# Kernel optimization log

Hardware: AMD Instinct MI355X
Metric: run time of the kernel (lower is better)

The kernel has to match this reference:

```python
import jax, jax.numpy as jnp
import numpy as np

D = 160          # SDF grid resolution (D1=D2=D3=D)
LEVEL = 0.0      # marching_cubes(-sdf, level=-0) == level 0 on s = -sdf
N_SMOOTH = 2
LAMBD = 1.0


def _extract_mesh_np():
    """Host-side isosurface extraction (mirrors the module's CPU round-trip).
    Uses marching tetrahedra (6-tet cube decomposition) in place of skimage's
    lewiner marching cubes; topo_correct (undefined in source) is identity.
    Returns (verts [V,3] f32 in normalized coords, faces [F,3] i32, edges [E,2] i32).
    """
    xs = np.arange(D, dtype=np.float32)
    X, Y, Z = np.meshgrid(xs, xs, xs, indexing='ij')
    ctr = (D - 1) / 2.0
    sdf = np.sqrt((X - ctr) ** 2 + (Y - ctr) ** 2 + (Z - ctr) ** 2) - 0.35 * D
    sdf = sdf + 3.0 * np.sin(0.20 * X) * np.sin(0.17 * Y) * np.sin(0.23 * Z)
    s = (-sdf).astype(np.float32)  # extract level-0 isosurface of -sdf
    sflat = s.ravel()
    Ng = D ** 3

    corner_off = [(0, 0, 0), (1, 0, 0), (1, 1, 0), (0, 1, 0),
                  (0, 0, 1), (1, 0, 1), (1, 1, 1), (0, 1, 1)]
    b = np.arange(D - 1)
    BX, BY, BZ = np.meshgrid(b, b, b, indexing='ij')
    BX, BY, BZ = BX.ravel(), BY.ravel(), BZ.ravel()
    gid8 = [((BX + dx) * D + (BY + dy)) * D + (BZ + dz) for dx, dy, dz in corner_off]
    val8 = [sflat[g] for g in gid8]

    TETS = [(0, 5, 1, 6), (0, 1, 2, 6), (0, 2, 3, 6),
            (0, 3, 7, 6), (0, 7, 4, 6), (0, 4, 5, 6)]
    TE = [(0, 1), (0, 2), (0, 3), (1, 2), (1, 3), (2, 3)]  # tet edges
    CASE_TRIS = {1: [(0, 1, 2)], 14: [(0, 1, 2)],
                 2: [(0, 3, 4)], 13: [(0, 3, 4)],
                 4: [(1, 3, 5)], 11: [(1, 3, 5)],
                 8: [(2, 4, 5)], 7: [(2, 4, 5)],
                 3: [(1, 3, 4), (1, 4, 2)], 12: [(1, 3, 4), (1, 4, 2)],
                 5: [(0, 3, 5), (0, 5, 2)], 10: [(0, 3, 5), (0, 5, 2)],
                 6: [(0, 4, 5), (0, 5, 1)], 9: [(0, 4, 5), (0, 5, 1)]}
    bitw = np.array([1, 2, 4, 8])

    tri_keys = []
    for tet in TETS:
        tv = np.stack([val8[c] for c in tet], 1)  # [Nc,4] corner values
        tg = np.stack([gid8[c] for c in tet], 1)  # [Nc,4] corner grid ids
        case = (tv < LEVEL).astype(np.int64) @ bitw
        for c, tris in CASE_TRIS.items():
            sel = np.nonzero(case == c)[0]
            if sel.size == 0:
                continue
            g = tg[sel]
            for tri in tris:
                cols = []
                for e in tri:
                    i, j = TE[e]
                    lo = np.minimum(g[:, i], g[:, j])
                    hi = np.maximum(g[:, i], g[:, j])
                    cols.append(lo * Ng + hi)  # canonical grid-edge key
                tri_keys.append(np.stack(cols, 1))
    tris = np.concatenate(tri_keys, 0)  # [F,3] edge keys
    uk, inv = np.unique(tris, return_inverse=True)
    faces = inv.reshape(-1, 3).astype(np.int32)
    ga = uk // Ng
    gb = uk % Ng
    pa = np.stack(np.unravel_index(ga, (D, D, D)), 1).astype(np.float32)
    pb = np.stack(np.unravel_index(gb, (D, D, D)), 1).astype(np.float32)
    sa = sflat[ga]
    sb = sflat[gb]
    t = ((LEVEL - sa) / (sb - sa)).astype(np.float32)
    verts = pa + t[:, None] * (pb - pa)
    verts = (2.0 * verts - np.float32(D)) / np.float32(D)  # (2v-[D1,D2,D3])/D
    e = np.concatenate([faces[:, [0, 1]], faces[:, [1, 2]], faces[:, [2, 0]]], 0)
    e = np.unique(np.sort(e, 1), axis=0).astype(np.int32)
    return verts.astype(np.float32), faces, e


def setup_inputs() -> dict:
    verts, faces, edges = _extract_mesh_np()
    return {
        'v': jnp.asarray(verts)[None],      # [1,V,3]
        'edges': jnp.asarray(edges),        # [E,2] unique undirected mesh edges
        'faces': jnp.asarray(faces)[None],  # [1,F,3]
    }


def reference(v, edges, faces):
    # Uniform laplacian smoothing: v <- v + lambd * (mean_neighbor(v) - v), x2
    V = v.shape[1]
    src = jnp.concatenate([edges[:, 0], edges[:, 1]])
    dst = jnp.concatenate([edges[:, 1], edges[:, 0]])
    x = v[0]
    deg = jax.ops.segment_sum(jnp.ones(src.shape[0], x.dtype), src, num_segments=V)
    inv_deg = 1.0 / jnp.maximum(deg, 1.0)
    for _ in range(N_SMOOTH):
        nbr = jax.ops.segment_sum(x[dst], src, num_segments=V)
        x = x + LAMBD * (nbr * inv_deg[:, None] - x)
    return x, faces[0]
```

## Files before the change

kernel.cpp:

```cpp
#include <hip/hip_runtime.h>
#include <stdint.h>

#define K_ELL 32
#define K_OVF 16
#define TBS   1024
#define RNG_LOG 11
#define RNG   2048
#define BAND  2048
#define RW    (RNG + BAND)
#define BS    256
#define UA    6
#define UN    6
#define UF    4

__global__ void prep_kernel(const int2* __restrict__ edges, int* __restrict__ offs_a,
                            int* __restrict__ cntN, int* __restrict__ cntF,
                            int* __restrict__ deg_ovf, int E, int V) {
    int i = blockIdx.x * blockDim.x + threadIdx.x;
    if (i <= E) {
        if (i < E) {
            int lo = (i == 0) ? 0 : edges[i - 1].x + 1;
            int hi = edges[i].x;
            for (int a = lo; a <= hi; a++) offs_a[a] = i;
        } else {
            for (int a = edges[E - 1].x + 1; a <= V; a++) offs_a[a] = E;
        }
    }
    if (i < V) deg_ovf[i] = 0;
    if (i <= RNG) cntF[i] = 0;
    if (i == 0) cntN[0] = 0;
}

__global__ __launch_bounds__(TBS) void build_kernel(
        const int2* __restrict__ edges, const int* __restrict__ offs_a,
        int* __restrict__ cntN, int* __restrict__ cntF, int* __restrict__ deg_ovf,
        int* __restrict__ adjN, int* __restrict__ adjF, int* __restrict__ adj_ovf,
        const int* __restrict__ faces, float* __restrict__ out_f,
        const float* __restrict__ v, float4* __restrict__ v4,
        int E, int V, int F3, int NBb) {
    if ((int)blockIdx.x >= NBb) {
        int t = (blockIdx.x - NBb) * TBS + threadIdx.x;
        int T = (gridDim.x - NBb) * TBS;
        if ((((uintptr_t)out_f | (uintptr_t)faces) & 15) == 0) {
            int n4 = F3 >> 2;
            const int4* f4 = (const int4*)faces;
            float4* o4 = (float4*)out_f;
            for (int j = t; j < n4; j += T) {
                int4 a = f4[j];
                o4[j] = make_float4((float)a.x, (float)a.y, (float)a.z, (float)a.w);
            }
            for (int j = (n4 << 2) + t; j < F3; j += T) out_f[j] = (float)faces[j];
        } else {
            for (int j = t; j < F3; j += T) out_f[j] = (float)faces[j];
        }
        if (((uintptr_t)v & 15) == 0) {
            const float4* vv = (const float4*)v;
            int n4v = V >> 2;
            for (int q = t; q < n4v; q += T) {
                float4 a = vv[3 * q], b = vv[3 * q + 1], c = vv[3 * q + 2];
                v4[4 * q + 0] = make_float4(a.x, a.y, a.z, 0.f);
                v4[4 * q + 1] = make_float4(a.w, b.x, b.y, 0.f);
                v4[4 * q + 2] = make_float4(b.z, b.w, c.x, 0.f);
                v4[4 * q + 3] = make_float4(c.y, c.z, c.w, 0.f);
            }
            for (int u = (n4v << 2) + t; u < V; u += T)
                v4[u] = make_float4(v[3 * u], v[3 * u + 1], v[3 * u + 2], 0.f);
        } else {
            for (int u = t; u < V; u += T)
                v4[u] = make_float4(v[3 * u], v[3 * u + 1], v[3 * u + 2], 0.f);
        }
        return;
    }
    __shared__ int cnt[RW];
    const int v0   = blockIdx.x << RNG_LOG;
    const int vEnd = min(v0 + RNG, V);
    for (int i = threadIdx.x; i < RW; i += TBS) cnt[i] = 0;
    const int eBeg = offs_a[v0];
    const int eEnd = offs_a[vEnd];
    __syncthreads();
    for (int i = eBeg + threadIdx.x; i < eEnd; i += TBS) {
        int2 e = edges[i];
        int rel = e.y - (v0 + 1);
        if (rel < RW) {
            int r = atomicAdd(&cnt[rel], 1);
            if (rel < RNG) { if (r < K_ELL) adjN[(size_t)r * V + e.y] = e.x; }
            else           { if (r < K_ELL) adjF[(size_t)r * V + e.y] = e.x; }
        } else {
            int r = atomicAdd(&deg_ovf[e.y], 1);
            if (r < K_OVF) adj_ovf[(size_t)r * V + e.y] = e.x;
        }
    }
    __syncthreads();
    for (int i = threadIdx.x; i < RW; i += TBS) {
        int u = v0 + 1 + i;
        if (u < V) {
            if (i < RNG) cntN[u] = cnt[i];
            else         cntF[u] = cnt[i];
        }
    }
}

template <bool PAD>
__global__ void gather_kernel(const float4* __restrict__ x4, const int2* __restrict__ edges,
                              const int* __restrict__ offs_a,
                              const int* __restrict__ cntN, const int* __restrict__ cntF,
                              const int* __restrict__ deg_ovf,
                              const int* __restrict__ adjN, const int* __restrict__ adjF,
                              const int* __restrict__ adj_ovf,
                              float* __restrict__ y, int V, int E) {
    int u = blockIdx.x * blockDim.x + threadIdx.x;
    if (u >= V) return;
    int aBeg = offs_a[u], aEnd = offs_a[u + 1];
    int cN = cntN[u], cF = cntF[u], dO = deg_ovf[u];
    int da = aEnd - aBeg;
    int kN = cN > K_ELL ? K_ELL : cN;
    int kF = cF > K_ELL ? K_ELL : cF;
    int gA[UA], gN[UN], gF[UF];
    #pragma unroll
    for (int j = 0; j < UA; ++j) gA[j] = edges[min(aBeg + j, E - 1)].y;
    #pragma unroll
    for (int k = 0; k < UN; ++k) gN[k] = adjN[(size_t)k * V + u];
    #pragma unroll
    for (int k = 0; k < UF; ++k) gF[k] = adjF[(size_t)k * V + u];
    float s0 = 0.f, s1 = 0.f, s2 = 0.f;
    #pragma unroll
    for (int j = 0; j < UA; ++j) {
        float m = (j < da) ? 1.f : 0.f;
        float4 p = x4[gA[j]];
        s0 += m * p.x; s1 += m * p.y; s2 += m * p.z;
    }
    for (int j = UA; j < da; ++j) {
        float4 p = x4[edges[aBeg + j].y];
        s0 += p.x; s1 += p.y; s2 += p.z;
    }
    #pragma unroll
    for (int k = 0; k < UN; ++k) {
        float m = (k < kN) ? 1.f : 0.f;
        float4 p = x4[(k < kN) ? gN[k] : 0];
        s0 += m * p.x; s1 += m * p.y; s2 += m * p.z;
    }
    for (int k = UN; k < kN; ++k) {
        float4 p = x4[adjN[(size_t)k * V + u]];
        s0 += p.x; s1 += p.y; s2 += p.z;
    }
    #pragma unroll
    for (int k = 0; k < UF; ++k) {
        float m = (k < kF) ? 1.f : 0.f;
        float4 p = x4[(k < kF) ? gF[k] : 0];
        s0 += m * p.x; s1 += m * p.y; s2 += m * p.z;
    }
    for (int k = UF; k < kF; ++k) {
        float4 p = x4[adjF[(size_t)k * V + u]];
        s0 += p.x; s1 += p.y; s2 += p.z;
    }
    int kO = dO > K_OVF ? K_OVF : dO;
    for (int k = 0; k < kO; ++k) {
        float4 p = x4[adj_ovf[(size_t)k * V + u]];
        s0 += p.x; s1 += p.y; s2 += p.z;
    }
    int d = da + cN + cF + dO;
    float inv = 1.0f / fmaxf((float)d, 1.0f);
    if (PAD) {
        ((float4*)y)[u] = make_float4(s0 * inv, s1 * inv, s2 * inv, 0.f);
    } else {
        y[3 * u + 0] = s0 * inv;
        y[3 * u + 1] = s1 * inv;
        y[3 * u + 2] = s2 * inv;
    }
}

extern "C" void kernel_launch(void* const* d_in, const int* in_sizes, int n_in,
                              void* d_out, int out_size, void* d_ws, size_t ws_size,
                              hipStream_t stream) {
    const float* v     = (const float*)d_in[0];
    const int2*  edges = (const int2*)d_in[1];
    const int*   faces = (const int*)d_in[2];

    const int V3 = in_sizes[0];
    const int V  = V3 / 3;
    const int E  = in_sizes[1] / 2;
    const int F3 = in_sizes[2];

    float* out_v = (float*)d_out;
    float* out_f = (float*)d_out + V3;

    float4* v4      = (float4*)d_ws;
    float4* x1      = v4 + V;
    int*    adjN    = (int*)(x1 + V);
    int*    adjF    = adjN + (size_t)K_ELL * V;
    int*    adj_ovf = adjF + (size_t)K_ELL * V;
    int*    offs_a  = adj_ovf + (size_t)K_OVF * V;
    int*    cntN    = offs_a + (V + 1);
    int*    cntF    = cntN + (V + 1);
    int*    deg_ovf = cntF + (V + 1);

    const int NBb = (V + RNG - 1) / RNG;
    const int copyElems = F3 > V ? F3 : V;
    const int NBc = (copyElems + TBS - 1) / TBS;
    const int gP  = (E + 1 + BS - 1) / BS;
    const int gV  = (V + BS - 1) / BS;

    prep_kernel<<<gP, BS, 0, stream>>>(edges, offs_a, cntN, cntF, deg_ovf, E, V);

    build_kernel<<<NBb + NBc, TBS, 0, stream>>>(edges, offs_a, cntN, cntF, deg_ovf,
                                                adjN, adjF, adj_ovf, faces, out_f,
                                                v, v4, E, V, F3, NBb);

    gather_kernel<true ><<<gV, BS, 0, stream>>>(v4, edges, offs_a, cntN, cntF, deg_ovf,
                                                adjN, adjF, adj_ovf, (float*)x1, V, E);
    gather_kernel<false><<<gV, BS, 0, stream>>>(x1, edges, offs_a, cntN, cntF, deg_ovf,
                                                adjN, adjF, adj_ovf, out_v, V, E);
}
```

Baseline: 86.52 us.

## Fuse prep into build with global atomics and stage vertex halo in LDS for gather

Drops the separate prep kernel. Offsets, faces conversion, vertex padding and adjacency construction now run in one grid-stride build kernel that uses global atomics on per-vertex counters, which a memset zeroes first. The gather kernels use 1024-thread blocks that stage a halo window of vertex positions in LDS (about 144KB) and serve in-window neighbours from there, falling back to global loads otherwise. The large LDS footprint cuts occupancy, and the global atomics may contend more than the old LDS counting.

```diff
diff --git a/kernel.cpp b/kernel.cpp
--- a/kernel.cpp
+++ b/kernel.cpp
@@ -3,130 +3,122 @@
 
 #define K_ELL 32
 #define K_OVF 16
-#define TBS   1024
-#define RNG_LOG 11
 #define RNG   2048
-#define BAND  2048
-#define RW    (RNG + BAND)
-#define BS    256
+#define RW    (RNG + RNG)
+#define BB    256
 #define UA    6
 #define UN    6
 #define UF    4
-
-__global__ void prep_kernel(const int2* __restrict__ edges, int* __restrict__ offs_a,
-                            int* __restrict__ cntN, int* __restrict__ cntF,
-                            int* __restrict__ deg_ovf, int E, int V) {
-    int i = blockIdx.x * blockDim.x + threadIdx.x;
-    if (i <= E) {
-        if (i < E) {
-            int lo = (i == 0) ? 0 : edges[i - 1].x + 1;
-            int hi = edges[i].x;
-            for (int a = lo; a <= hi; a++) offs_a[a] = i;
-        } else {
-            for (int a = edges[E - 1].x + 1; a <= V; a++) offs_a[a] = E;
-        }
-    }
-    if (i < V) deg_ovf[i] = 0;
-    if (i <= RNG) cntF[i] = 0;
-    if (i == 0) cntN[0] = 0;
-}
-
-__global__ __launch_bounds__(TBS) void build_kernel(
-        const int2* __restrict__ edges, const int* __restrict__ offs_a,
+#define GBS   1024
+#define HALO  4096
+#define SPAN  (GBS + 2 * HALO)
+#define SMEM_STG (SPAN * (int)sizeof(float4))
+
+__global__ __launch_bounds__(BB) void build_kernel(
+        const int2* __restrict__ edges, int* __restrict__ offs_a,
         int* __restrict__ cntN, int* __restrict__ cntF, int* __restrict__ deg_ovf,
         int* __restrict__ adjN, int* __restrict__ adjF, int* __restrict__ adj_ovf,
         const int* __restrict__ faces, float* __restrict__ out_f,
         const float* __restrict__ v, float4* __restrict__ v4,
-        int E, int V, int F3, int NBb) {
-    if ((int)blockIdx.x >= NBb) {
-        int t = (blockIdx.x - NBb) * TBS + threadIdx.x;
-        int T = (gridDim.x - NBb) * TBS;
-        if ((((uintptr_t)out_f | (uintptr_t)faces) & 15) == 0) {
-            int n4 = F3 >> 2;
-            const int4* f4 = (const int4*)faces;
-            float4* o4 = (float4*)out_f;
-            for (int j = t; j < n4; j += T) {
-                int4 a = f4[j];
-                o4[j] = make_float4((float)a.x, (float)a.y, (float)a.z, (float)a.w);
-            }
-            for (int j = (n4 << 2) + t; j < F3; j += T) out_f[j] = (float)faces[j];
-        } else {
-            for (int j = t; j < F3; j += T) out_f[j] = (float)faces[j];
-        }
-        if (((uintptr_t)v & 15) == 0) {
-            const float4* vv = (const float4*)v;
-            int n4v = V >> 2;
-            for (int q = t; q < n4v; q += T) {
-                float4 a = vv[3 * q], b = vv[3 * q + 1], c = vv[3 * q + 2];
-                v4[4 * q + 0] = make_float4(a.x, a.y, a.z, 0.f);
-                v4[4 * q + 1] = make_float4(a.w, b.x, b.y, 0.f);
-                v4[4 * q + 2] = make_float4(b.z, b.w, c.x, 0.f);
-                v4[4 * q + 3] = make_float4(c.y, c.z, c.w, 0.f);
-            }
-            for (int u = (n4v << 2) + t; u < V; u += T)
-                v4[u] = make_float4(v[3 * u], v[3 * u + 1], v[3 * u + 2], 0.f);
-        } else {
-            for (int u = t; u < V; u += T)
-                v4[u] = make_float4(v[3 * u], v[3 * u + 1], v[3 * u + 2], 0.f);
-        }
-        return;
-    }
-    __shared__ int cnt[RW];
-    const int v0   = blockIdx.x << RNG_LOG;
-    const int vEnd = min(v0 + RNG, V);
-    for (int i = threadIdx.x; i < RW; i += TBS) cnt[i] = 0;
-    const int eBeg = offs_a[v0];
-    const int eEnd = offs_a[vEnd];
-    __syncthreads();
-    for (int i = eBeg + threadIdx.x; i < eEnd; i += TBS) {
+        int E, int V, int F3) {
+    const int t = (int)blockIdx.x * BB + (int)threadIdx.x;
+    const int T = (int)gridDim.x * BB;
+    for (int i = t; i < E; i += T) {
         int2 e = edges[i];
-        int rel = e.y - (v0 + 1);
-        if (rel < RW) {
-            int r = atomicAdd(&cnt[rel], 1);
-            if (rel < RNG) { if (r < K_ELL) adjN[(size_t)r * V + e.y] = e.x; }
-            else           { if (r < K_ELL) adjF[(size_t)r * V + e.y] = e.x; }
+        int rel = e.y - (e.x & ~(RNG - 1)) - 1;
+        if (rel < RNG) {
+            int r = atomicAdd(&cntN[e.y], 1);
+            if (r < K_ELL) adjN[(size_t)r * V + e.y] = e.x;
+        } else if (rel < RW) {
+            int r = atomicAdd(&cntF[e.y], 1);
+            if (r < K_ELL) adjF[(size_t)r * V + e.y] = e.x;
         } else {
             int r = atomicAdd(&deg_ovf[e.y], 1);
             if (r < K_OVF) adj_ovf[(size_t)r * V + e.y] = e.x;
         }
     }
+    for (int i = t; i <= E; i += T) {
+        if (i < E) {
+            int lo = (i == 0) ? 0 : edges[i - 1].x + 1;
+            int hi = edges[i].x;
+            for (int a = lo; a <= hi; ++a) offs_a[a] = i;
+        } else {
+            int lo = (E > 0) ? edges[E - 1].x + 1 : 0;
+            for (int a = lo; a <= V; ++a) offs_a[a] = E;
+        }
+    }
+    if ((((uintptr_t)out_f | (uintptr_t)faces) & 15) == 0) {
+        int n4 = F3 >> 2;
+        const int4* f4 = (const int4*)faces;
+        float4* o4 = (float4*)out_f;
+        for (int j = t; j < n4; j += T) {
+            int4 a = f4[j];
+            o4[j] = make_float4((float)a.x, (float)a.y, (float)a.z, (float)a.w);
+        }
+        for (int j = (n4 << 2) + t; j < F3; j += T) out_f[j] = (float)faces[j];
+    } else {
+        for (int j = t; j < F3; j += T) out_f[j] = (float)faces[j];
+    }
+    if (((uintptr_t)v & 15) == 0) {
+        const float4* vv = (const float4*)v;
+        int n4v = V >> 2;
+        for (int q = t; q < n4v; q += T) {
+            float4 a = vv[3 * q], b = vv[3 * q + 1], c = vv[3 * q + 2];
+            v4[4 * q + 0] = make_float4(a.x, a.y, a.z, 0.f);
+            v4[4 * q + 1] = make_float4(a.w, b.x, b.y, 0.f);
+            v4[4 * q + 2] = make_float4(b.z, b.w, c.x, 0.f);
+            v4[4 * q + 3] = make_float4(c.y, c.z, c.w, 0.f);
+        }
+        for (int u = (n4v << 2) + t; u < V; u += T)
+            v4[u] = make_float4(v[3 * u], v[3 * u + 1], v[3 * u + 2], 0.f);
+    } else {
+        for (int u = t; u < V; u += T)
+            v4[u] = make_float4(v[3 * u], v[3 * u + 1], v[3 * u + 2], 0.f);
+    }
+}
+
+template <bool PAD>
+__global__ __launch_bounds__(GBS) void gather_staged(
+        const float4* __restrict__ x4, const int2* __restrict__ edges,
+        const int* __restrict__ offs_a,
+        const int* __restrict__ cntN, const int* __restrict__ cntF,
+        const int* __restrict__ deg_ovf,
+        const int* __restrict__ adjN, const int* __restrict__ adjF,
+        const int* __restrict__ adj_ovf,
+        float* __restrict__ y, int V, int E) {
+    extern __shared__ float4 tile[];
+    const int c0   = (int)blockIdx.x * GBS;
+    const int base = c0 - HALO;
+    const int u    = c0 + (int)threadIdx.x;
+    int aBeg = 0, da = 0, cN = 0, cF = 0, dO = 0;
+    int gA[UA], gN[UN], gF[UF];
+    if (u < V) {
+        aBeg = offs_a[u];
+        int aEnd = offs_a[u + 1];
+        da = aEnd - aBeg;
+        cN = cntN[u]; cF = cntF[u]; dO = deg_ovf[u];
+        #pragma unroll
+        for (int j = 0; j < UA; ++j) gA[j] = edges[min(aBeg + j, E - 1)].y;
+        #pragma unroll
+        for (int k = 0; k < UN; ++k) gN[k] = adjN[(size_t)k * V + u];
+        #pragma unroll
+        for (int k = 0; k < UF; ++k) gF[k] = adjF[(size_t)k * V + u];
+    }
+    for (int s = (int)threadIdx.x; s < SPAN; s += GBS) {
+        int g = base + s;
+        tile[s] = (g >= 0 && g < V) ? x4[g] : make_float4(0.f, 0.f, 0.f, 0.f);
+    }
     __syncthreads();
-    for (int i = threadIdx.x; i < RW; i += TBS) {
-        int u = v0 + 1 + i;
-        if (u < V) {
-            if (i < RNG) cntN[u] = cnt[i];
-            else         cntF[u] = cnt[i];
-        }
-    }
-}
-
-template <bool PAD>
-__global__ void gather_kernel(const float4* __restrict__ x4, const int2* __restrict__ edges,
-                              const int* __restrict__ offs_a,
-                              const int* __restrict__ cntN, const int* __restrict__ cntF,
-                              const int* __restrict__ deg_ovf,
-                              const int* __restrict__ adjN, const int* __restrict__ adjF,
-                              const int* __restrict__ adj_ovf,
-                              float* __restrict__ y, int V, int E) {
-    int u = blockIdx.x * blockDim.x + threadIdx.x;
     if (u >= V) return;
-    int aBeg = offs_a[u], aEnd = offs_a[u + 1];
-    int cN = cntN[u], cF = cntF[u], dO = deg_ovf[u];
-    int da = aEnd - aBeg;
     int kN = cN > K_ELL ? K_ELL : cN;
     int kF = cF > K_ELL ? K_ELL : cF;
-    int gA[UA], gN[UN], gF[UF];
-    #pragma unroll
-    for (int j = 0; j < UA; ++j) gA[j] = edges[min(aBeg + j, E - 1)].y;
-    #pragma unroll
-    for (int k = 0; k < UN; ++k) gN[k] = adjN[(size_t)k * V + u];
-    #pragma unroll
-    for (int k = 0; k < UF; ++k) gF[k] = adjF[(size_t)k * V + u];
     float s0 = 0.f, s1 = 0.f, s2 = 0.f;
     #pragma unroll
     for (int j = 0; j < UA; ++j) {
+        int g = (j < da) ? gA[j] : u;
         float m = (j < da) ? 1.f : 0.f;
-        float4 p = x4[gA[j]];
+        unsigned r = (unsigned)(g - base);
+        float4 p = (r < (unsigned)SPAN) ? tile[r] : x4[g];
         s0 += m * p.x; s1 += m * p.y; s2 += m * p.z;
     }
     for (int j = UA; j < da; ++j) {
@@ -135,8 +127,10 @@
     }
     #pragma unroll
     for (int k = 0; k < UN; ++k) {
+        int g = (k < kN) ? gN[k] : u;
         float m = (k < kN) ? 1.f : 0.f;
-        float4 p = x4[(k < kN) ? gN[k] : 0];
+        unsigned r = (unsigned)(g - base);
+        float4 p = (r < (unsigned)SPAN) ? tile[r] : x4[g];
         s0 += m * p.x; s1 += m * p.y; s2 += m * p.z;
     }
     for (int k = UN; k < kN; ++k) {
@@ -145,8 +139,10 @@
     }
     #pragma unroll
     for (int k = 0; k < UF; ++k) {
+        int g = (k < kF) ? gF[k] : u;
         float m = (k < kF) ? 1.f : 0.f;
-        float4 p = x4[(k < kF) ? gF[k] : 0];
+        unsigned r = (unsigned)(g - base);
+        float4 p = (r < (unsigned)SPAN) ? tile[r] : x4[g];
         s0 += m * p.x; s1 += m * p.y; s2 += m * p.z;
     }
     for (int k = UF; k < kF; ++k) {
@@ -194,20 +190,22 @@
     int*    cntF    = cntN + (V + 1);
     int*    deg_ovf = cntF + (V + 1);
 
-    const int NBb = (V + RNG - 1) / RNG;
-    const int copyElems = F3 > V ? F3 : V;
-    const int NBc = (copyElems + TBS - 1) / TBS;
-    const int gP  = (E + 1 + BS - 1) / BS;
-    const int gV  = (V + BS - 1) / BS;
-
-    prep_kernel<<<gP, BS, 0, stream>>>(edges, offs_a, cntN, cntF, deg_ovf, E, V);
-
-    build_kernel<<<NBb + NBc, TBS, 0, stream>>>(edges, offs_a, cntN, cntF, deg_ovf,
-                                                adjN, adjF, adj_ovf, faces, out_f,
-                                                v, v4, E, V, F3, NBb);
-
-    gather_kernel<true ><<<gV, BS, 0, stream>>>(v4, edges, offs_a, cntN, cntF, deg_ovf,
-                                                adjN, adjF, adj_ovf, (float*)x1, V, E);
-    gather_kernel<false><<<gV, BS, 0, stream>>>(x1, edges, offs_a, cntN, cntF, deg_ovf,
-                                                adjN, adjF, adj_ovf, out_v, V, E);
+    (void)hipMemsetAsync(cntN, 0, (size_t)(3 * V + 2) * sizeof(int), stream);
+
+    int maxWork = E + 1;
+    if (F3 > maxWork) maxWork = F3;
+    if (V > maxWork)  maxWork = V;
+    int gB = (maxWork + BB - 1) / BB;
+    if (gB > 2048) gB = 2048;
+    build_kernel<<<gB, BB, 0, stream>>>(edges, offs_a, cntN, cntF, deg_ovf,
+                                        adjN, adjF, adj_ovf, faces, out_f,
+                                        v, v4, E, V, F3);
+
+    int gS = (V + GBS - 1) / GBS;
+    gather_staged<true ><<<gS, GBS, SMEM_STG, stream>>>(
+        v4, edges, offs_a, cntN, cntF, deg_ovf, adjN, adjF, adj_ovf,
+        (float*)x1, V, E);
+    gather_staged<false><<<gS, GBS, SMEM_STG, stream>>>(
+        x1, edges, offs_a, cntN, cntF, deg_ovf, adjN, adjF, adj_ovf,
+        out_v, V, E);
 }
```

Measured after the change: 104.1 us. 20.3% more time.
